# Performance work log

Hardware: AMD Instinct MI355X
Metric: run time of the kernel (lower is better)

The kernel has to match this reference:

```python
import jax, jax.numpy as jnp
import numpy as np

B, N, D, L = 16, 100, 1024, 2000


def setup_inputs() -> dict:
    key = jax.random.key(0)
    ks = jax.random.split(key, 9)
    s = 1.0 / np.sqrt(D)
    return {
        "feature": jax.random.normal(ks[0], (B, N, D), dtype=jnp.float32),
        "graph": jax.random.randint(ks[1], (B, N, N), 0, L),
        "W0": jax.random.normal(ks[2], (D, D), dtype=jnp.float32) * s,
        "W1": jax.random.normal(ks[3], (D, D), dtype=jnp.float32) * s,
        "bias": jax.random.uniform(ks[4], (L, D), dtype=jnp.float32, minval=-s, maxval=s),
        "dp_Wa": jax.random.normal(ks[5], (D, D), dtype=jnp.float32) * s,
        "dp_ba": jax.random.normal(ks[6], (D,), dtype=jnp.float32) * s,
        "dp_Wb": jax.random.normal(ks[7], (D, D), dtype=jnp.float32) * s,
        "dp_bb": jax.random.normal(ks[8], (D,), dtype=jnp.float32) * s,
        "get_alpha": 0,
    }


def reference(feature, graph, W0, W1, bias, dp_Wa, dp_ba, dp_Wb, dp_bb, get_alpha):
    # ---- DirectedGraphConv.conv ----
    adj = (graph != 0).astype(feature.dtype)                     # [B,N,N]
    out = feature + feature @ W0.T + feature @ W1.T              # [B,N,D]
    out = out + jnp.take(bias, graph, axis=0).sum(axis=2)        # label-embedding gather+sum over neighbors
    # ---- relation_alpha: DotProduct(feature, feature) ----
    a = feature @ dp_Wa.T + dp_ba                                # [B,N,D]
    b = feature @ dp_Wb.T + dp_bb                                # [B,N,D]
    alpha = jnp.einsum('bik,bjk->bij', a, b)                     # [B,N,N]
    alpha = jnp.maximum(alpha, 0.0)                              # alpha[alpha<0]=0
    alpha = jnp.einsum('bij,bjk->bik', adj, alpha)               # bmm(adj, alpha)
    alpha = jax.nn.softmax(alpha, axis=1)                        # Softmax(dim=1)
    out = jnp.einsum('bij,bjk->bik', alpha, out)                 # bmm(alpha, output)
    if get_alpha:
        return (out, alpha)
    return out
```

## Files before the change

kernel.cpp:

```cpp
#include <hip/hip_runtime.h>
#include <stdint.h>

#define B_   16
#define N_   100
#define D_   1024
#define L_   2000
#define M_   1600
#define KP   2048

#define RCAP 24
#define ZMAX 2400
#define TC   12

typedef __bf16 bf16x8 __attribute__((ext_vector_type(8)));
typedef float  f32x4  __attribute__((ext_vector_type(4)));

__device__ __forceinline__ void gl_lds16(const __bf16* g, __bf16* l) {
    __builtin_amdgcn_global_load_lds(
        (const __attribute__((address_space(1))) void*)g,
        (__attribute__((address_space(3))) void*)l, 16, 0, 0);
}


__global__ void __launch_bounds__(256)
k_prep(const float* __restrict__ f,
       const float* __restrict__ W0, const float* __restrict__ W1,
       const float* __restrict__ Wa, const float* __restrict__ Wb,
       const float* __restrict__ bias, const int* __restrict__ graph,
       __bf16* __restrict__ fb, __bf16* __restrict__ wcat,
       __bf16* __restrict__ biasBT, __bf16* __restrict__ cnt) {
    int bid = blockIdx.x, t = threadIdx.x;
    __shared__ float lds[32][33];
    __shared__ unsigned int hist[KP];

    if (bid < 2336) {
        int i = bid * 256 + t;
        union { __bf16 h[8]; uint4 u; } pk;
        if (i < 204800) {
            long base = (long)i * 8;
            const float4* p = (const float4*)(f + base);
            float4 x = p[0], y = p[1];
            pk.h[0]=(__bf16)x.x; pk.h[1]=(__bf16)x.y; pk.h[2]=(__bf16)x.z; pk.h[3]=(__bf16)x.w;
            pk.h[4]=(__bf16)y.x; pk.h[5]=(__bf16)y.y; pk.h[6]=(__bf16)y.z; pk.h[7]=(__bf16)y.w;
            ((uint4*)fb)[i] = pk.u;
        } else {
            int j = i - 204800;
            long base = (long)j * 8;
            long seg = base >> 20;
            long off = base & ((1l << 20) - 1);
            if (seg == 0) {
                const float4* p0 = (const float4*)(W0 + off);
                const float4* p1 = (const float4*)(W1 + off);
                float4 a0 = p0[0], a1 = p0[1], b0 = p1[0], b1 = p1[1];
                pk.h[0]=(__bf16)(a0.x+b0.x); pk.h[1]=(__bf16)(a0.y+b0.y);
                pk.h[2]=(__bf16)(a0.z+b0.z); pk.h[3]=(__bf16)(a0.w+b0.w);
                pk.h[4]=(__bf16)(a1.x+b1.x); pk.h[5]=(__bf16)(a1.y+b1.y);
                pk.h[6]=(__bf16)(a1.z+b1.z); pk.h[7]=(__bf16)(a1.w+b1.w);
            } else {
                const float* src = (seg == 1) ? Wa : Wb;
                const float4* p = (const float4*)(src + off);
                float4 x = p[0], y = p[1];
                pk.h[0]=(__bf16)x.x; pk.h[1]=(__bf16)x.y; pk.h[2]=(__bf16)x.z; pk.h[3]=(__bf16)x.w;
                pk.h[4]=(__bf16)y.x; pk.h[5]=(__bf16)y.y; pk.h[6]=(__bf16)y.z; pk.h[7]=(__bf16)y.w;
            }
            ((uint4*)wcat)[j] = pk.u;
        }
    } else if (bid < 4384) {
        int tb = bid - 2336;
        int lt = tb >> 5, dt = tb & 31;
        int l0 = lt * 32, d0 = dt * 32;
        int r = t >> 3, cq = (t & 7) * 4;
        float4 v = make_float4(0.f, 0.f, 0.f, 0.f);
        if (l0 + r < L_) v = *(const float4*)(bias + (long)(l0 + r) * D_ + d0 + cq);
        lds[r][cq]=v.x; lds[r][cq+1]=v.y; lds[r][cq+2]=v.z; lds[r][cq+3]=v.w;
        __syncthreads();
        union { __bf16 h[4]; uint2 u; } pk;
        #pragma unroll
        for (int q = 0; q < 4; ++q) pk.h[q] = (__bf16)lds[cq + q][r];
        *(uint2*)(biasBT + (long)(d0 + r) * KP + l0 + cq) = pk.u;
    } else {
        int m = bid - 4384;
        for (int k = t; k < KP; k += 256) hist[k] = 0u;
        __syncthreads();
        if (t < N_) atomicAdd(&hist[graph[(long)m * N_ + t]], 1u);
        __syncthreads();
        for (int k = t; k < KP; k += 256)
            cnt[(long)m * KP + k] = (__bf16)(float)hist[k];
    }
}


#define BM 64
#define BN 128
#define BK 64

__global__ void __launch_bounds__(256)
k_gemmAll(const __bf16* __restrict__ fb, const __bf16* __restrict__ wcat,
          const __bf16* __restrict__ cnt, const __bf16* __restrict__ biasBT,
          const float* __restrict__ feat, const float* __restrict__ ba,
          const float* __restrict__ bbias,
          float* __restrict__ out0, float* __restrict__ aB, float* __restrict__ bB,
          float* __restrict__ out0add) {
    __shared__ __align__(16) __bf16 As[BM * BK];
    __shared__ __align__(16) __bf16 Bs[BN * BK];
    int t = threadIdx.x;
    int pid = blockIdx.x;
    int lane = t & 63, wave = t >> 6;
    int wr = wave & 1, wc = wave >> 1;
    int lrow = lane & 15, quad = lane >> 4;

    bool isMain = pid < 600;
    int bm, bn, lda, K;
    const __bf16 *Ag, *Bg;
    if (isMain) {
        int v = (pid & 7) * 75 + (pid >> 3);
        bn = v / 25; bm = v % 25;
        Ag = fb   + (long)(bm * BM) * D_;
        Bg = wcat + (long)(bn * BN) * D_;
        lda = D_; K = D_;
    } else {
        int q = pid - 600;
        int v = (q & 7) * 25 + (q >> 3);
        bm = v >> 3; bn = v & 7;
        Ag = cnt    + (long)(bm * BM) * KP;
        Bg = biasBT + (long)(bn * BN) * KP;
        lda = KP; K = KP;
    }

    f32x4 acc[2][4] = {};
    for (int k0 = 0; k0 < K; k0 += BK) {
        #pragma unroll
        for (int pi = 0; pi < 2; ++pi) {
            int p = pi * 256 + t, row = p >> 3, c = (p & 7) ^ (row & 7);
            gl_lds16(Ag + (long)row * lda + k0 + c * 8, As + p * 8);
        }
        #pragma unroll
        for (int pi = 0; pi < 4; ++pi) {
            int p = pi * 256 + t, row = p >> 3, c = (p & 7) ^ (row & 7);
            gl_lds16(Bg + (long)row * lda + k0 + c * 8, Bs + p * 8);
        }
        __syncthreads();
        #pragma unroll
        for (int ks = 0; ks < 2; ++ks) {
            bf16x8 af[2], bf[4];
            #pragma unroll
            for (int i = 0; i < 2; ++i) {
                int r = wr * 32 + i * 16 + lrow;
                int slot = r * 8 + (((ks << 2) | quad) ^ (r & 7));
                af[i] = *(const bf16x8*)(As + slot * 8);
            }
            #pragma unroll
            for (int j = 0; j < 4; ++j) {
                int r = wc * 64 + j * 16 + lrow;
                int slot = r * 8 + (((ks << 2) | quad) ^ (r & 7));
                bf[j] = *(const bf16x8*)(Bs + slot * 8);
            }
            #pragma unroll
            for (int i = 0; i < 2; ++i)
                #pragma unroll
                for (int j = 0; j < 4; ++j)
                    acc[i][j] = __builtin_amdgcn_mfma_f32_16x16x32_bf16(af[i], bf[j], acc[i][j], 0, 0, 0);
        }
        __syncthreads();
    }

    if (isMain) {
        int nbase = bn * BN;
        int seg = bn >> 3;
        #pragma unroll
        for (int i = 0; i < 2; ++i) {
            int gm0 = bm * BM + wr * 32 + i * 16 + quad * 4;
            #pragma unroll
            for (int j = 0; j < 4; ++j) {
                int col = (nbase + wc * 64 + j * 16 + lrow) & 1023;
                #pragma unroll
                for (int r = 0; r < 4; ++r) {
                    long m = gm0 + r;
                    float v = acc[i][j][r];
                    if (seg == 0)      out0[m * D_ + col] = v + feat[m * D_ + col];
                    else if (seg == 1) aB[m * D_ + col]   = v + ba[col];
                    else               bB[m * D_ + col]   = v + bbias[col];
                }
            }
        }
    } else {
        #pragma unroll
        for (int i = 0; i < 2; ++i) {
            int gm0 = bm * BM + wr * 32 + i * 16 + quad * 4;
            #pragma unroll
            for (int j = 0; j < 4; ++j) {
                int col = bn * BN + wc * 64 + j * 16 + lrow;
                #pragma unroll
                for (int r = 0; r < 4; ++r) {
                    long m = gm0 + r;
                    out0add[m * D_ + col] = acc[i][j][r];
                }
            }
        }
    }
}


__global__ void __launch_bounds__(256)
k_alpha(const int* __restrict__ graph, const float* __restrict__ aB,
        const float* __restrict__ bB, float* __restrict__ wl, float* __restrict__ cwG) {
    __shared__ int rowCnt[N_], rowOff[N_], rowRank[N_];
    __shared__ int ndvS, totZS;
    __shared__ int zjL[ZMAX];
    __shared__ short prL[ZMAX];
    __shared__ float corrL[RCAP][4];
    __shared__ float wred[4][4];

    int pid = blockIdx.x;
    int b = pid / 25, kc = pid - b * 25;
    int t = threadIdx.x, lane = t & 63, wave = t >> 6;

    const int* g = graph + (long)b * N_ * N_;
    if (t < N_) {
        int c = 0;
        for (int j = 0; j < N_; ++j) if (g[t * N_ + j] == 0) ++c;
        rowCnt[t] = c;
    }
    if (t < RCAP * 4) corrL[t >> 2][t & 3] = 0.f;
    __syncthreads();
    if (t == 0) {
        int off = 0, rank = 0;
        for (int i = 0; i < N_; ++i) {
            if (rowCnt[i] > 0 && rank < RCAP) {
                rowRank[i] = rank; rowOff[i] = off; off += rowCnt[i]; ++rank;
            } else rowRank[i] = -1;
        }
        ndvS = rank; totZS = off;
    }
    __syncthreads();
    if (t < N_ && rowRank[t] >= 0) {
        int pos = rowOff[t], r = rowRank[t];
        for (int j = 0; j < N_; ++j)
            if (g[t * N_ + j] == 0) { zjL[pos] = j; prL[pos] = (short)r; ++pos; }
    }
    __syncthreads();
    int Z = totZS, ndv = ndvS;

    int k0 = kc * 4;
    float4 bv[4];
    #pragma unroll
    for (int kk = 0; kk < 4; ++kk)
        bv[kk] = *(const float4*)(bB + ((long)(b * N_ + k0 + kk)) * D_ + t * 4);

    for (int q = 0; q < Z; ++q) {
        const float* ar = aB + ((long)(b * N_ + zjL[q])) * D_;
        float4 av = *(const float4*)(ar + t * 4);
        float s[4];
        #pragma unroll
        for (int kk = 0; kk < 4; ++kk)
            s[kk] = av.x * bv[kk].x + av.y * bv[kk].y + av.z * bv[kk].z + av.w * bv[kk].w;
        #pragma unroll
        for (int off = 32; off > 0; off >>= 1)
            #pragma unroll
            for (int kk = 0; kk < 4; ++kk) s[kk] += __shfl_xor(s[kk], off);
        if (lane == 0) { wred[wave][0]=s[0]; wred[wave][1]=s[1]; wred[wave][2]=s[2]; wred[wave][3]=s[3]; }
        __syncthreads();
        if (t < 4) {
            float v = wred[0][t] + wred[1][t] + wred[2][t] + wred[3][t];
            corrL[prL[q]][t] += fmaxf(v, 0.f);
        }
        __syncthreads();
    }

    if (t < 4) {
        int k = k0 + t;
        float denom = (float)(N_ - ndv);
        for (int r = 0; r < ndv; ++r) {
            float e = __expf(-corrL[r][t]);
            corrL[r][t] = e;
            denom += e;
        }
        float w = 1.f / denom;
        wl[b * N_ + k] = w;
        for (int r = 0; r < ndv; ++r)
            cwG[((long)b * RCAP + r) * N_ + k] = corrL[r][t] * w;
    }
}


__global__ void __launch_bounds__(256)
k_mix(const int* __restrict__ graph, const float* __restrict__ wl,
      const float* __restrict__ cwG, const float* __restrict__ out0,
      const float* __restrict__ out0add, float* __restrict__ out) {
    int b = blockIdx.x, dq = blockIdx.y;
    int t = threadIdx.x, c4 = t & 63, q = t >> 6;
    int d0 = dq * 256;
    __shared__ int hasZ[N_], mapL[N_], ndvS;
    __shared__ float wT[TC][N_];
    __shared__ f32x4 parts[4][TC][64];

    const int* g = graph + (long)b * N_ * N_;
    if (t < N_) {
        int z = 0;
        for (int j = 0; j < N_; ++j) if (g[t * N_ + j] == 0) { z = 1; break; }
        hasZ[t] = z;
    }
    __syncthreads();
    if (t < N_) {
        int rank = 0;
        for (int i = 0; i < t; ++i) rank += hasZ[i];
        mapL[t] = (hasZ[t] && rank < RCAP) ? 1 + rank : 0;
    }
    if (t == 0) {
        int n = 0;
        for (int i = 0; i < N_; ++i) n += hasZ[i];
        ndvS = min(n, RCAP);
    }
    __syncthreads();
    int ndv = ndvS, ntask = ndv + 1;

    const float* o0 = out0    + (long)b * N_ * D_ + d0;
    const float* oa = out0add + (long)b * N_ * D_ + d0;
    for (int cb = 0; cb < ntask; cb += TC) {
        for (int idx = t; idx < TC * N_; idx += 256) {
            int rr = idx / N_, j = idx - rr * N_;
            int task = cb + rr;
            float v = 0.f;
            if (task == 0)         v = wl[b * N_ + j];
            else if (task <= ndv)  v = cwG[((long)b * RCAP + task - 1) * N_ + j];
            wT[rr][j] = v;
        }
        __syncthreads();
        f32x4 acc[TC] = {};
        for (int j = q * 25; j < q * 25 + 25; ++j) {
            f32x4 v = *(const f32x4*)(o0 + (long)j * D_ + c4 * 4)
                    + *(const f32x4*)(oa + (long)j * D_ + c4 * 4);
            #pragma unroll
            for (int rr = 0; rr < TC; ++rr) acc[rr] += wT[rr][j] * v;
        }
        #pragma unroll
        for (int rr = 0; rr < TC; ++rr) parts[q][rr][c4] = acc[rr];
        __syncthreads();
        for (int i = q * 25; i < q * 25 + 25; ++i) {
            int task = mapL[i];
            if (task >= cb && task < cb + TC) {
                int rr = task - cb;
                f32x4 s = parts[0][rr][c4] + parts[1][rr][c4]
                        + parts[2][rr][c4] + parts[3][rr][c4];
                *(f32x4*)(out + ((long)(b * N_ + i)) * D_ + d0 + c4 * 4) = s;
            }
        }
        __syncthreads();
    }
}


extern "C" void kernel_launch(void* const* d_in, const int* in_sizes, int n_in,
                              void* d_out, int out_size, void* d_ws, size_t ws_size,
                              hipStream_t stream) {
    const float* feature = (const float*)d_in[0];
    const int*   graph   = (const int*)d_in[1];
    const float* W0      = (const float*)d_in[2];
    const float* W1      = (const float*)d_in[3];
    const float* bias    = (const float*)d_in[4];
    const float* dp_Wa   = (const float*)d_in[5];
    const float* dp_ba   = (const float*)d_in[6];
    const float* dp_Wb   = (const float*)d_in[7];
    const float* dp_bb   = (const float*)d_in[8];
    float* out = (float*)d_out;

    char* w = (char*)d_ws;
    __bf16* fb16    = (__bf16*)(w);
    __bf16* wcat    = (__bf16*)(w + 3276800);
    __bf16* cnt     = (__bf16*)(w + 9568256);
    __bf16* biasBT  = (__bf16*)(w + 16121856);
    float*  out0    = (float*)(w + 20316160);
    float*  aB      = (float*)(w + 26869760);
    float*  bB      = (float*)(w + 33423360);
    float*  wl      = (float*)(w + 39976960);
    float*  cwG     = (float*)(w + 39983360);
    float*  out0add = (float*)(w + 40136960);

    k_prep<<<5984, 256, 0, stream>>>(feature, W0, W1, dp_Wa, dp_Wb, bias, graph,
                                     fb16, wcat, biasBT, cnt);
    k_gemmAll<<<800, 256, 0, stream>>>(fb16, wcat, cnt, biasBT, feature, dp_ba, dp_bb,
                                       out0, aB, bB, out0add);
    k_alpha<<<400, 256, 0, stream>>>(graph, aB, bB, wl, cwG);
    k_mix<<<dim3(B_, 4), 256, 0, stream>>>(graph, wl, cwG, out0, out0add, out);
}
```

Measured before the change: 176.5 us.

## Split-K the fused GEMMs into two halves and sum partials in consumers

Doubles the GEMM grid from 800 to 1600 blocks by splitting the K dimension in two, with each half writing its own partial buffer. The downstream alpha and mix kernels now read both partials and add them, which removes any atomics or extra reduction kernel. The histogram-to-bf16 store is also vectorized into 16-byte writes. The trade-off is more global memory traffic, since partial outputs are written and re-read twice, and a larger workspace.

```diff
diff --git a/kernel.cpp b/kernel.cpp
--- a/kernel.cpp
+++ b/kernel.cpp
@@ -84,8 +84,10 @@
         __syncthreads();
         if (t < N_) atomicAdd(&hist[graph[(long)m * N_ + t]], 1u);
         __syncthreads();
-        for (int k = t; k < KP; k += 256)
-            cnt[(long)m * KP + k] = (__bf16)(float)hist[k];
+        union { __bf16 h[8]; uint4 u; } pk;
+        #pragma unroll
+        for (int q = 0; q < 8; ++q) pk.h[q] = (__bf16)(float)hist[t * 8 + q];
+        ((uint4*)(cnt + (long)m * KP))[t] = pk.u;
     }
 }
 
@@ -99,8 +101,10 @@
           const __bf16* __restrict__ cnt, const __bf16* __restrict__ biasBT,
           const float* __restrict__ feat, const float* __restrict__ ba,
           const float* __restrict__ bbias,
-          float* __restrict__ out0, float* __restrict__ aB, float* __restrict__ bB,
-          float* __restrict__ out0add) {
+          float* __restrict__ out0A, float* __restrict__ out0B,
+          float* __restrict__ aBA, float* __restrict__ aBB,
+          float* __restrict__ bBA, float* __restrict__ bBB,
+          float* __restrict__ out0addA, float* __restrict__ out0addB) {
     __shared__ __align__(16) __bf16 As[BM * BK];
     __shared__ __align__(16) __bf16 Bs[BN * BK];
     int t = threadIdx.x;
@@ -109,26 +113,30 @@
     int wr = wave & 1, wc = wave >> 1;
     int lrow = lane & 15, quad = lane >> 4;
 
-    bool isMain = pid < 600;
-    int bm, bn, lda, K;
+    bool isMain = pid < 1200;
+    int bm, bn, s, lda, kBeg, kEnd;
     const __bf16 *Ag, *Bg;
     if (isMain) {
-        int v = (pid & 7) * 75 + (pid >> 3);
-        bn = v / 25; bm = v % 25;
+        int v = (pid & 7) * 150 + (pid >> 3);
+        bn = v / 50;
+        int rem = v - bn * 50;
+        bm = rem >> 1; s = rem & 1;
         Ag = fb   + (long)(bm * BM) * D_;
         Bg = wcat + (long)(bn * BN) * D_;
-        lda = D_; K = D_;
+        lda = D_; kBeg = s * 512; kEnd = kBeg + 512;
     } else {
-        int q = pid - 600;
-        int v = (q & 7) * 25 + (q >> 3);
-        bm = v >> 3; bn = v & 7;
+        int q = pid - 1200;
+        int v = (q & 7) * 50 + (q >> 3);
+        bm = v >> 4;
+        int rem = v & 15;
+        bn = rem >> 1; s = rem & 1;
         Ag = cnt    + (long)(bm * BM) * KP;
         Bg = biasBT + (long)(bn * BN) * KP;
-        lda = KP; K = KP;
+        lda = KP; kBeg = s * 1024; kEnd = kBeg + 1024;
     }
 
     f32x4 acc[2][4] = {};
-    for (int k0 = 0; k0 < K; k0 += BK) {
+    for (int k0 = kBeg; k0 < kEnd; k0 += BK) {
         #pragma unroll
         for (int pi = 0; pi < 2; ++pi) {
             int p = pi * 256 + t, row = p >> 3, c = (p & 7) ^ (row & 7);
@@ -165,21 +173,27 @@
     }
 
     if (isMain) {
-        int nbase = bn * BN;
         int seg = bn >> 3;
         #pragma unroll
         for (int i = 0; i < 2; ++i) {
             int gm0 = bm * BM + wr * 32 + i * 16 + quad * 4;
             #pragma unroll
             for (int j = 0; j < 4; ++j) {
-                int col = (nbase + wc * 64 + j * 16 + lrow) & 1023;
+                int col = (bn & 7) * BN + wc * 64 + j * 16 + lrow;
                 #pragma unroll
                 for (int r = 0; r < 4; ++r) {
                     long m = gm0 + r;
                     float v = acc[i][j][r];
-                    if (seg == 0)      out0[m * D_ + col] = v + feat[m * D_ + col];
-                    else if (seg == 1) aB[m * D_ + col]   = v + ba[col];
-                    else               bB[m * D_ + col]   = v + bbias[col];
+                    long idx = m * D_ + col;
+                    if (s == 0) {
+                        if (seg == 0)      out0A[idx] = v + feat[idx];
+                        else if (seg == 1) aBA[idx]   = v + ba[col];
+                        else               bBA[idx]   = v + bbias[col];
+                    } else {
+                        if (seg == 0)      out0B[idx] = v;
+                        else if (seg == 1) aBB[idx]   = v;
+                        else               bBB[idx]   = v;
+                    }
                 }
             }
         }
@@ -193,7 +207,8 @@
                 #pragma unroll
                 for (int r = 0; r < 4; ++r) {
                     long m = gm0 + r;
-                    out0add[m * D_ + col] = acc[i][j][r];
+                    if (s == 0) out0addA[m * D_ + col] = acc[i][j][r];
+                    else        out0addB[m * D_ + col] = acc[i][j][r];
                 }
             }
         }
@@ -202,8 +217,10 @@
 
 
 __global__ void __launch_bounds__(256)
-k_alpha(const int* __restrict__ graph, const float* __restrict__ aB,
-        const float* __restrict__ bB, float* __restrict__ wl, float* __restrict__ cwG) {
+k_alpha(const int* __restrict__ graph,
+        const float* __restrict__ aBA, const float* __restrict__ aBB,
+        const float* __restrict__ bBA, const float* __restrict__ bBB,
+        float* __restrict__ wl, float* __restrict__ cwG) {
     __shared__ int rowCnt[N_], rowOff[N_], rowRank[N_];
     __shared__ int ndvS, totZS;
     __shared__ int zjL[ZMAX];
@@ -244,12 +261,18 @@
     int k0 = kc * 4;
     float4 bv[4];
     #pragma unroll
-    for (int kk = 0; kk < 4; ++kk)
-        bv[kk] = *(const float4*)(bB + ((long)(b * N_ + k0 + kk)) * D_ + t * 4);
+    for (int kk = 0; kk < 4; ++kk) {
+        long off = ((long)(b * N_ + k0 + kk)) * D_ + t * 4;
+        float4 x = *(const float4*)(bBA + off);
+        float4 y = *(const float4*)(bBB + off);
+        bv[kk] = make_float4(x.x + y.x, x.y + y.y, x.z + y.z, x.w + y.w);
+    }
 
     for (int q = 0; q < Z; ++q) {
-        const float* ar = aB + ((long)(b * N_ + zjL[q])) * D_;
-        float4 av = *(const float4*)(ar + t * 4);
+        long aoff = ((long)(b * N_ + zjL[q])) * D_ + t * 4;
+        float4 a1 = *(const float4*)(aBA + aoff);
+        float4 a2 = *(const float4*)(aBB + aoff);
+        float4 av = make_float4(a1.x + a2.x, a1.y + a2.y, a1.z + a2.z, a1.w + a2.w);
         float s[4];
         #pragma unroll
         for (int kk = 0; kk < 4; ++kk)
@@ -285,8 +308,10 @@
 
 __global__ void __launch_bounds__(256)
 k_mix(const int* __restrict__ graph, const float* __restrict__ wl,
-      const float* __restrict__ cwG, const float* __restrict__ out0,
-      const float* __restrict__ out0add, float* __restrict__ out) {
+      const float* __restrict__ cwG,
+      const float* __restrict__ out0A, const float* __restrict__ out0B,
+      const float* __restrict__ out0addA, const float* __restrict__ out0addB,
+      float* __restrict__ out) {
     int b = blockIdx.x, dq = blockIdx.y;
     int t = threadIdx.x, c4 = t & 63, q = t >> 6;
     int d0 = dq * 256;
@@ -314,8 +339,11 @@
     __syncthreads();
     int ndv = ndvS, ntask = ndv + 1;
 
-    const float* o0 = out0    + (long)b * N_ * D_ + d0;
-    const float* oa = out0add + (long)b * N_ * D_ + d0;
+    long base = (long)b * N_ * D_ + d0;
+    const float* o1 = out0A    + base;
+    const float* o2 = out0B    + base;
+    const float* o3 = out0addA + base;
+    const float* o4 = out0addB + base;
     for (int cb = 0; cb < ntask; cb += TC) {
         for (int idx = t; idx < TC * N_; idx += 256) {
             int rr = idx / N_, j = idx - rr * N_;
@@ -328,8 +356,9 @@
         __syncthreads();
         f32x4 acc[TC] = {};
         for (int j = q * 25; j < q * 25 + 25; ++j) {
-            f32x4 v = *(const f32x4*)(o0 + (long)j * D_ + c4 * 4)
-                    + *(const f32x4*)(oa + (long)j * D_ + c4 * 4);
+            long o = (long)j * D_ + c4 * 4;
+            f32x4 v = *(const f32x4*)(o1 + o) + *(const f32x4*)(o2 + o)
+                    + *(const f32x4*)(o3 + o) + *(const f32x4*)(o4 + o);
             #pragma unroll
             for (int rr = 0; rr < TC; ++rr) acc[rr] += wT[rr][j] * v;
         }
@@ -365,21 +394,27 @@
     float* out = (float*)d_out;
 
     char* w = (char*)d_ws;
-    __bf16* fb16    = (__bf16*)(w);
-    __bf16* wcat    = (__bf16*)(w + 3276800);
-    __bf16* cnt     = (__bf16*)(w + 9568256);
-    __bf16* biasBT  = (__bf16*)(w + 16121856);
-    float*  out0    = (float*)(w + 20316160);
-    float*  aB      = (float*)(w + 26869760);
-    float*  bB      = (float*)(w + 33423360);
-    float*  wl      = (float*)(w + 39976960);
-    float*  cwG     = (float*)(w + 39983360);
-    float*  out0add = (float*)(w + 40136960);
+    __bf16* fb16     = (__bf16*)(w);
+    __bf16* wcat     = (__bf16*)(w + 3276800);
+    __bf16* cnt      = (__bf16*)(w + 9568256);
+    __bf16* biasBT   = (__bf16*)(w + 16121856);
+    float*  out0A    = (float*)(w + 20316160);
+    float*  out0B    = (float*)(w + 26869760);
+    float*  aBA      = (float*)(w + 33423360);
+    float*  aBB      = (float*)(w + 39976960);
+    float*  bBA      = (float*)(w + 46530560);
+    float*  bBB      = (float*)(w + 53084160);
+    float*  out0addA = (float*)(w + 59637760);
+    float*  out0addB = (float*)(w + 66191360);
+    float*  wl       = (float*)(w + 72744960);
+    float*  cwG      = (float*)(w + 72751360);
 
     k_prep<<<5984, 256, 0, stream>>>(feature, W0, W1, dp_Wa, dp_Wb, bias, graph,
                                      fb16, wcat, biasBT, cnt);
-    k_gemmAll<<<800, 256, 0, stream>>>(fb16, wcat, cnt, biasBT, feature, dp_ba, dp_bb,
-                                       out0, aB, bB, out0add);
-    k_alpha<<<400, 256, 0, stream>>>(graph, aB, bB, wl, cwG);
-    k_mix<<<dim3(B_, 4), 256, 0, stream>>>(graph, wl, cwG, out0, out0add, out);
-}
+    k_gemmAll<<<1600, 256, 0, stream>>>(fb16, wcat, cnt, biasBT, feature, dp_ba, dp_bb,
+                                        out0A, out0B, aBA, aBB, bBA, bBB,
+                                        out0addA, out0addB);
+    k_alpha<<<400, 256, 0, stream>>>(graph, aBA, aBB, bBA, bBB, wl, cwG);
+    k_mix<<<dim3(B_, 4), 256, 0, stream>>>(graph, wl, cwG, out0A, out0B,
+                                           out0addA, out0addB, out);
+}
```

Measured after the change: 179.7 us. Within noise of the previous version (+1.9%).
